# Performance work log

Hardware: AMD Instinct MI355X
Metric: run time of the kernel (lower is better)

Reference implementation:

```python
import jax, jax.numpy as jnp
from jax import lax
import numpy as np

SMOOTH = 0.015
EPS = 1e-9


def setup_inputs() -> dict:
    key = jax.random.key(0)
    k_x, k_a, k_p, k_b = jax.random.split(key, 4)
    B, F, T, C = 64, 256, 2048, 1
    x = jax.random.uniform(k_x, (B, F, T, C), dtype=jnp.float32)  # nonneg energies
    # learned scalars ~ N(1.0, 0.1) as in tf.random_normal_initializer(mean=1.0, stddev=0.1)
    alpha = 1.0 + 0.1 * jax.random.normal(k_a, (1,), dtype=jnp.float32)
    power = 1.0 + 0.1 * jax.random.normal(k_p, (1,), dtype=jnp.float32)
    bias = 1.0 + 0.1 * jax.random.normal(k_b, (1,), dtype=jnp.float32)
    return {"x": x, "alpha": alpha, "power": power, "bias": bias}


def _smoother(x):
    # x: [B, F, T, C]; IIR: M_0 = s*x_0, M_t = (1-s)*M_{t-1} + s*x_t
    xt = jnp.moveaxis(x, 2, 0)  # [T, B, F, C]
    m0 = SMOOTH * xt[0]

    def step(m_prev, xi):
        m = (1.0 - SMOOTH) * m_prev + SMOOTH * xi
        return m, m

    _, ms = lax.scan(step, m0, xt[1:])
    M = jnp.concatenate([m0[None], ms], axis=0)  # [T, B, F, C]
    return jnp.moveaxis(M, 0, 2)  # [B, F, T, C]


def reference(x, alpha, power, bias):
    M = _smoother(x)
    return jnp.power(x / jnp.power(EPS + M, alpha) + bias, power) - jnp.power(bias, power)
```

## Files before the change

### kernel.cpp

```cpp
#include <hip/hip_runtime.h>


#define T_LEN 2048
#define NCH   8
#define CHUNK 256

__device__ __forceinline__ float fast_exp2(float x) { return __builtin_amdgcn_exp2f(x); }
__device__ __forceinline__ float fast_log2(float x) { return __builtin_amdgcn_logf(x); }
__device__ __forceinline__ float readlane63(float v) {
    return __int_as_float(__builtin_amdgcn_readlane(__float_as_int(v), 63));
}

__global__ __launch_bounds__(256, 4) void pcen_kernel(
    const float* __restrict__ x,
    const float* __restrict__ alpha_p,
    const float* __restrict__ power_p,
    const float* __restrict__ bias_p,
    float* __restrict__ out)
{
    const int wave = threadIdx.x >> 6;
    const int lane = threadIdx.x & 63;
    const int row  = (blockIdx.x << 2) | wave;

    const float alpha = alpha_p[0];
    const float power = power_p[0];
    const float bias  = bias_p[0];

    const float A = 0.985f;
    const float S = 0.015f;
    const float A2 = A * A;
    const float f4 = A2 * A2;

    const float* xr  = x   + (size_t)row * T_LEN + 4 * lane;
    float*       orw = out + (size_t)row * T_LEN + 4 * lane;

    float4 v[NCH];
#pragma unroll
    for (int c = 0; c < NCH; ++c)
        v[c] = *reinterpret_cast<const float4*>(xr + c * CHUNK);

    float fl = 1.0f, t = f4;
#pragma unroll
    for (int b = 1; b < 64; b <<= 1) {
        fl = (lane & b) ? fl * t : fl;
        t *= t;
    }
    const float F = t;

    float s[NCH];
#pragma unroll
    for (int c = 0; c < NCH; ++c) {
        float m = 0.0f;
        m = fmaf(A, m, S * v[c].x);
        m = fmaf(A, m, S * v[c].y);
        m = fmaf(A, m, S * v[c].z);
        m = fmaf(A, m, S * v[c].w);
        s[c] = m;
    }

    {
        float g = f4;
#pragma unroll
        for (int d = 1; d < 64; d <<= 1) {
#pragma unroll
            for (int c = 0; c < NCH; ++c) {
                const float so = __shfl_up(s[c], d, 64);
                if (lane >= d) s[c] = fmaf(g, so, s[c]);
            }
            g *= g;
        }
    }

    float e[NCH];
#pragma unroll
    for (int c = 0; c < NCH; ++c) {
        e[c] = __shfl_up(s[c], 1, 64);
        if (lane == 0) e[c] = 0.0f;
    }

    const float bias_pow = fast_exp2(power * fast_log2(bias));
    const float nalpha   = -alpha;

    float R = 0.0f;
#pragma unroll
    for (int c = 0; c < NCH; ++c) {
        const float s63 = readlane63(s[c]);
        float M = fmaf(fl, R, e[c]);
        R = fmaf(F, R, s63);

        float4 r;
#pragma unroll
        for (int j = 0; j < 4; ++j) {
            const float xj = (j == 0) ? v[c].x : (j == 1) ? v[c].y
                           : (j == 2) ? v[c].z : v[c].w;
            M = fmaf(A, M, S * xj);
            const float den = 1e-9f + M;
            const float tt  = fmaf(xj, fast_exp2(nalpha * fast_log2(den)), bias);
            const float rr  = fast_exp2(power * fast_log2(tt)) - bias_pow;
            if (j == 0) r.x = rr; else if (j == 1) r.y = rr;
            else if (j == 2) r.z = rr; else r.w = rr;
        }
        *reinterpret_cast<float4*>(orw + c * CHUNK) = r;
    }
}

extern "C" void kernel_launch(void* const* d_in, const int* in_sizes, int n_in,
                              void* d_out, int out_size, void* d_ws, size_t ws_size,
                              hipStream_t stream) {
    const float* x       = (const float*)d_in[0];
    const float* alpha_p = (const float*)d_in[1];
    const float* power_p = (const float*)d_in[2];
    const float* bias_p  = (const float*)d_in[3];
    float* out           = (float*)d_out;

    const int nrows  = in_sizes[0] / T_LEN;
    const int blocks = nrows / 4;

    pcen_kernel<<<blocks, 256, 0, stream>>>(x, alpha_p, power_p, bias_p, out);
}
```

Baseline: 236.0 us.

## Process four rows per wave with software-prefetched loads and nontemporal stores

Each wave now handles four consecutive rows in a loop and prefetches the next row's data into registers while it computes the current row, so load latency overlaps with the scan and transcendental work. Output stores become nontemporal to avoid polluting the cache. The grid shrinks fourfold and register pressure roughly doubles for the input buffers, which may reduce occupancy or parallelism.

```diff
diff --git a/kernel.cpp b/kernel.cpp
--- a/kernel.cpp
+++ b/kernel.cpp
@@ -4,6 +4,9 @@
 #define T_LEN 2048
 #define NCH   8
 #define CHUNK 256
+#define RPW   4
+
+typedef float vfloat4 __attribute__((ext_vector_type(4)));
 
 __device__ __forceinline__ float fast_exp2(float x) { return __builtin_amdgcn_exp2f(x); }
 __device__ __forceinline__ float fast_log2(float x) { return __builtin_amdgcn_logf(x); }
@@ -20,24 +23,19 @@
 {
     const int wave = threadIdx.x >> 6;
     const int lane = threadIdx.x & 63;
-    const int row  = (blockIdx.x << 2) | wave;
+    const int gw   = (blockIdx.x << 2) | wave;
 
     const float alpha = alpha_p[0];
     const float power = power_p[0];
     const float bias  = bias_p[0];
 
-    const float A = 0.985f;
-    const float S = 0.015f;
+    const float A  = 0.985f;
+    const float S  = 0.015f;
     const float A2 = A * A;
     const float f4 = A2 * A2;
 
-    const float* xr  = x   + (size_t)row * T_LEN + 4 * lane;
-    float*       orw = out + (size_t)row * T_LEN + 4 * lane;
-
-    float4 v[NCH];
-#pragma unroll
-    for (int c = 0; c < NCH; ++c)
-        v[c] = *reinterpret_cast<const float4*>(xr + c * CHUNK);
+    const float* xr  = x   + (size_t)gw * (RPW * T_LEN) + 4 * lane;
+    float*       orw = out + (size_t)gw * (RPW * T_LEN) + 4 * lane;
 
     float fl = 1.0f, t = f4;
 #pragma unroll
@@ -47,60 +45,75 @@
     }
     const float F = t;
 
-    float s[NCH];
-#pragma unroll
-    for (int c = 0; c < NCH; ++c) {
-        float m = 0.0f;
-        m = fmaf(A, m, S * v[c].x);
-        m = fmaf(A, m, S * v[c].y);
-        m = fmaf(A, m, S * v[c].z);
-        m = fmaf(A, m, S * v[c].w);
-        s[c] = m;
-    }
-
-    {
-        float g = f4;
-#pragma unroll
-        for (int d = 1; d < 64; d <<= 1) {
-#pragma unroll
-            for (int c = 0; c < NCH; ++c) {
-                const float so = __shfl_up(s[c], d, 64);
-                if (lane >= d) s[c] = fmaf(g, so, s[c]);
-            }
-            g *= g;
-        }
-    }
-
-    float e[NCH];
-#pragma unroll
-    for (int c = 0; c < NCH; ++c) {
-        e[c] = __shfl_up(s[c], 1, 64);
-        if (lane == 0) e[c] = 0.0f;
-    }
-
     const float bias_pow = fast_exp2(power * fast_log2(bias));
     const float nalpha   = -alpha;
 
-    float R = 0.0f;
+    float4 vc[NCH], vn[NCH];
+
 #pragma unroll
-    for (int c = 0; c < NCH; ++c) {
-        const float s63 = readlane63(s[c]);
-        float M = fmaf(fl, R, e[c]);
-        R = fmaf(F, R, s63);
+    for (int c = 0; c < NCH; ++c)
+        vc[c] = *reinterpret_cast<const float4*>(xr + c * CHUNK);
 
-        float4 r;
+#pragma unroll 1
+    for (int r = 0; r < RPW; ++r) {
+        if (r + 1 < RPW) {
 #pragma unroll
-        for (int j = 0; j < 4; ++j) {
-            const float xj = (j == 0) ? v[c].x : (j == 1) ? v[c].y
-                           : (j == 2) ? v[c].z : v[c].w;
-            M = fmaf(A, M, S * xj);
-            const float den = 1e-9f + M;
-            const float tt  = fmaf(xj, fast_exp2(nalpha * fast_log2(den)), bias);
-            const float rr  = fast_exp2(power * fast_log2(tt)) - bias_pow;
-            if (j == 0) r.x = rr; else if (j == 1) r.y = rr;
-            else if (j == 2) r.z = rr; else r.w = rr;
+            for (int c = 0; c < NCH; ++c)
+                vn[c] = *reinterpret_cast<const float4*>(
+                            xr + (size_t)(r + 1) * T_LEN + c * CHUNK);
         }
-        *reinterpret_cast<float4*>(orw + c * CHUNK) = r;
+
+        float s[NCH];
+#pragma unroll
+        for (int c = 0; c < NCH; ++c) {
+            float m = 0.0f;
+            m = fmaf(A, m, S * vc[c].x);
+            m = fmaf(A, m, S * vc[c].y);
+            m = fmaf(A, m, S * vc[c].z);
+            m = fmaf(A, m, S * vc[c].w);
+            s[c] = m;
+        }
+
+        {
+            float g = f4;
+#pragma unroll
+            for (int d = 1; d < 64; d <<= 1) {
+#pragma unroll
+                for (int c = 0; c < NCH; ++c) {
+                    const float so = __shfl_up(s[c], d, 64);
+                    if (lane >= d) s[c] = fmaf(g, so, s[c]);
+                }
+                g *= g;
+            }
+        }
+
+        float R = 0.0f;
+#pragma unroll
+        for (int c = 0; c < NCH; ++c) {
+            float e = __shfl_up(s[c], 1, 64);
+            if (lane == 0) e = 0.0f;
+            const float s63 = readlane63(s[c]);
+            float M = fmaf(fl, R, e);
+            R = fmaf(F, R, s63);
+
+            vfloat4 w;
+#pragma unroll
+            for (int j = 0; j < 4; ++j) {
+                const float xj = (j == 0) ? vc[c].x : (j == 1) ? vc[c].y
+                               : (j == 2) ? vc[c].z : vc[c].w;
+                M = fmaf(A, M, S * xj);
+                const float den = 1e-9f + M;
+                const float tt  = fmaf(xj, fast_exp2(nalpha * fast_log2(den)), bias);
+                w[j] = fast_exp2(power * fast_log2(tt)) - bias_pow;
+            }
+            __builtin_nontemporal_store(
+                w, reinterpret_cast<vfloat4*>(orw + (size_t)r * T_LEN + c * CHUNK));
+        }
+
+        if (r + 1 < RPW) {
+#pragma unroll
+            for (int c = 0; c < NCH; ++c) vc[c] = vn[c];
+        }
     }
 }
 
@@ -114,7 +127,7 @@
     float* out           = (float*)d_out;
 
     const int nrows  = in_sizes[0] / T_LEN;
-    const int blocks = nrows / 4;
+    const int blocks = nrows / (4 * RPW);
 
     pcen_kernel<<<blocks, 256, 0, stream>>>(x, alpha_p, power_p, bias_p, out);
 }
```

Measured after the change: 243.9 us. 3.4% more time.

## Process eight rows per wave with double-buffered global-to-LDS async loads

Applied to the files above, without the earlier changes.

Each wave now handles eight rows in a loop instead of one, and prefetches the next two rows from global memory into LDS with direct global_load_lds instructions. Manual vmcnt/lgkmcnt waits create a double-buffered pipeline so loads overlap the scan and transcendental math. The grid shrinks by a factor of eight and occupancy hints drop, which risks fewer waves to hide latency. The hand-written waitcnt values are also fragile if the compiler reorders or adds memory operations.

```diff
diff --git a/kernel.cpp b/kernel.cpp
--- a/kernel.cpp
+++ b/kernel.cpp
@@ -1,9 +1,12 @@
 #include <hip/hip_runtime.h>
 
 
-#define T_LEN 2048
-#define NCH   8
-#define CHUNK 256
+#define T_LEN  2048
+#define NCH    8
+#define CHUNK  256
+#define RPW    8
+#define ROWB   T_LEN
+#define WSLICE (2 * T_LEN)
 
 __device__ __forceinline__ float fast_exp2(float x) { return __builtin_amdgcn_exp2f(x); }
 __device__ __forceinline__ float fast_log2(float x) { return __builtin_amdgcn_logf(x); }
@@ -11,97 +14,122 @@
     return __int_as_float(__builtin_amdgcn_readlane(__float_as_int(v), 63));
 }
 
-__global__ __launch_bounds__(256, 4) void pcen_kernel(
+__global__ __launch_bounds__(256, 2) void pcen_kernel(
     const float* __restrict__ x,
     const float* __restrict__ alpha_p,
     const float* __restrict__ power_p,
     const float* __restrict__ bias_p,
     float* __restrict__ out)
 {
+    __shared__ float lds[4 * WSLICE];
+
     const int wave = threadIdx.x >> 6;
     const int lane = threadIdx.x & 63;
-    const int row  = (blockIdx.x << 2) | wave;
+    const int gw   = (blockIdx.x << 2) | wave;
+
+    float* const lbase = &lds[wave * WSLICE];
 
     const float alpha = alpha_p[0];
     const float power = power_p[0];
     const float bias  = bias_p[0];
 
-    const float A = 0.985f;
-    const float S = 0.015f;
+    const float A  = 0.985f;
+    const float S  = 0.015f;
     const float A2 = A * A;
     const float f4 = A2 * A2;
 
-    const float* xr  = x   + (size_t)row * T_LEN + 4 * lane;
-    float*       orw = out + (size_t)row * T_LEN + 4 * lane;
-
-    float4 v[NCH];
-#pragma unroll
-    for (int c = 0; c < NCH; ++c)
-        v[c] = *reinterpret_cast<const float4*>(xr + c * CHUNK);
+    const float* const xw = x   + (size_t)gw * (RPW * T_LEN);
+    float*       const ow = out + (size_t)gw * (RPW * T_LEN) + 4 * lane;
 
     float fl = 1.0f, t = f4;
 #pragma unroll
-    for (int b = 1; b < 64; b <<= 1) {
-        fl = (lane & b) ? fl * t : fl;
-        t *= t;
-    }
+    for (int b = 1; b < 64; b <<= 1) { fl = (lane & b) ? fl * t : fl; t *= t; }
     const float F = t;
-
-    float s[NCH];
-#pragma unroll
-    for (int c = 0; c < NCH; ++c) {
-        float m = 0.0f;
-        m = fmaf(A, m, S * v[c].x);
-        m = fmaf(A, m, S * v[c].y);
-        m = fmaf(A, m, S * v[c].z);
-        m = fmaf(A, m, S * v[c].w);
-        s[c] = m;
-    }
-
-    {
-        float g = f4;
-#pragma unroll
-        for (int d = 1; d < 64; d <<= 1) {
-#pragma unroll
-            for (int c = 0; c < NCH; ++c) {
-                const float so = __shfl_up(s[c], d, 64);
-                if (lane >= d) s[c] = fmaf(g, so, s[c]);
-            }
-            g *= g;
-        }
-    }
-
-    float e[NCH];
-#pragma unroll
-    for (int c = 0; c < NCH; ++c) {
-        e[c] = __shfl_up(s[c], 1, 64);
-        if (lane == 0) e[c] = 0.0f;
-    }
 
     const float bias_pow = fast_exp2(power * fast_log2(bias));
     const float nalpha   = -alpha;
 
-    float R = 0.0f;
+#define ISSUE_ROW(i, b)                                                         \
+    {                                                                           \
+        const float* gp = xw + (size_t)(i) * T_LEN + 4 * lane;                  \
+        float* lp = lbase + (b) * ROWB;                                         \
+        _Pragma("unroll")                                                       \
+        for (int c = 0; c < NCH; ++c) {                                         \
+            __builtin_amdgcn_global_load_lds(                                   \
+                (const __attribute__((address_space(1))) void*)(gp + c * CHUNK),\
+                (__attribute__((address_space(3))) void*)(lp + c * CHUNK),      \
+                16, 0, 0);                                                      \
+        }                                                                       \
+    }
+
+    ISSUE_ROW(0, 0);
+    ISSUE_ROW(1, 1);
+
+#pragma unroll 1
+    for (int i = 0; i < RPW; ++i) {
+        const int cur = i & 1;
+
+        if (i == 0) asm volatile("s_waitcnt vmcnt(8)" ::: "memory");
+        else        asm volatile("s_waitcnt vmcnt(16)" ::: "memory");
+
+        float4 v[NCH];
+        const float* lb = lbase + cur * ROWB + 4 * lane;
 #pragma unroll
-    for (int c = 0; c < NCH; ++c) {
-        const float s63 = readlane63(s[c]);
-        float M = fmaf(fl, R, e[c]);
-        R = fmaf(F, R, s63);
+        for (int c = 0; c < NCH; ++c)
+            v[c] = *reinterpret_cast<const float4*>(lb + c * CHUNK);
 
-        float4 r;
+        asm volatile("s_waitcnt lgkmcnt(0)" ::: "memory");
+        if (i + 2 < RPW) ISSUE_ROW(i + 2, cur);
+
+        float s[NCH];
 #pragma unroll
-        for (int j = 0; j < 4; ++j) {
-            const float xj = (j == 0) ? v[c].x : (j == 1) ? v[c].y
-                           : (j == 2) ? v[c].z : v[c].w;
-            M = fmaf(A, M, S * xj);
-            const float den = 1e-9f + M;
-            const float tt  = fmaf(xj, fast_exp2(nalpha * fast_log2(den)), bias);
-            const float rr  = fast_exp2(power * fast_log2(tt)) - bias_pow;
-            if (j == 0) r.x = rr; else if (j == 1) r.y = rr;
-            else if (j == 2) r.z = rr; else r.w = rr;
+        for (int c = 0; c < NCH; ++c) {
+            float m = 0.0f;
+            m = fmaf(A, m, S * v[c].x);
+            m = fmaf(A, m, S * v[c].y);
+            m = fmaf(A, m, S * v[c].z);
+            m = fmaf(A, m, S * v[c].w);
+            s[c] = m;
         }
-        *reinterpret_cast<float4*>(orw + c * CHUNK) = r;
+
+        {
+            float g = f4;
+#pragma unroll
+            for (int d = 1; d < 64; d <<= 1) {
+#pragma unroll
+                for (int c = 0; c < NCH; ++c) {
+                    const float so = __shfl_up(s[c], d, 64);
+                    if (lane >= d) s[c] = fmaf(g, so, s[c]);
+                }
+                g *= g;
+            }
+        }
+
+        float R = 0.0f;
+#pragma unroll
+        for (int c = 0; c < NCH; ++c) {
+            float e = __shfl_up(s[c], 1, 64);
+            if (lane == 0) e = 0.0f;
+            const float s63 = readlane63(s[c]);
+            float M = fmaf(fl, R, e);
+            R = fmaf(F, R, s63);
+
+            float4 r;
+#pragma unroll
+            for (int j = 0; j < 4; ++j) {
+                const float xj = (j == 0) ? v[c].x : (j == 1) ? v[c].y
+                               : (j == 2) ? v[c].z : v[c].w;
+                M = fmaf(A, M, S * xj);
+                const float den = 1e-9f + M;
+                const float tt  = fmaf(xj, fast_exp2(nalpha * fast_log2(den)), bias);
+                const float rr  = fast_exp2(power * fast_log2(tt)) - bias_pow;
+                if (j == 0) r.x = rr; else if (j == 1) r.y = rr;
+                else if (j == 2) r.z = rr; else r.w = rr;
+            }
+            *reinterpret_cast<float4*>(ow + (size_t)i * T_LEN + c * CHUNK) = r;
+        }
     }
+#undef ISSUE_ROW
 }
 
 extern "C" void kernel_launch(void* const* d_in, const int* in_sizes, int n_in,
@@ -114,7 +142,7 @@
     float* out           = (float*)d_out;
 
     const int nrows  = in_sizes[0] / T_LEN;
-    const int blocks = nrows / 4;
+    const int blocks = nrows / (4 * RPW);
 
     pcen_kernel<<<blocks, 256, 0, stream>>>(x, alpha_p, power_p, bias_p, out);
 }
```

Result: slower. 245.0 us (+3.8%).
